# Optimization experiments

Measured on AMD Instinct MI355X. Metric: run time of the kernel, lower is better.

The kernel has to match this reference:

```python
import jax, jax.numpy as jnp
import numpy as np
import math

N = 50000
E = 800000
HID = 128
HEADS = 8
DK = HID // HEADS
EPS_LN = 1e-5


def setup_inputs() -> dict:
    key = jax.random.key(0)
    ks = jax.random.split(key, 20)
    s = 1.0 / math.sqrt(HID)
    inp = {
        'x': jax.random.normal(ks[0], (N, HID), jnp.float32),
        'Wq': jax.random.normal(ks[1], (HID, HID), jnp.float32) * s,
        'bq': jnp.zeros((HID,), jnp.float32),
        'Wk': jax.random.normal(ks[2], (HID, HID), jnp.float32) * s,
        'bk': jnp.zeros((HID,), jnp.float32),
        'Wv': jax.random.normal(ks[3], (HID, HID), jnp.float32) * s,
        'bv': jnp.zeros((HID,), jnp.float32),
        'Wo': jax.random.normal(ks[4], (HID, HID), jnp.float32) * s,
        'bo': jnp.zeros((HID,), jnp.float32),
        'ln1_g': jnp.ones((HID,), jnp.float32),
        'ln1_b': jnp.zeros((HID,), jnp.float32),
        'W1': jax.random.normal(ks[5], (HID, 4 * HID), jnp.float32) * s,
        'b1': jnp.zeros((4 * HID,), jnp.float32),
        'W2': jax.random.normal(ks[6], (4 * HID, HID), jnp.float32) * (0.5 * s),
        'b2': jnp.zeros((HID,), jnp.float32),
        'ln2_g': jnp.ones((HID,), jnp.float32),
        'ln2_b': jnp.zeros((HID,), jnp.float32),
        'edge_index': jax.random.randint(ks[7], (2, E), 0, N, jnp.int64 if jax.config.jax_enable_x64 else jnp.int32),
    }
    return inp


def _layer_norm(x, g, b):
    mu = jnp.mean(x, axis=-1, keepdims=True)
    var = jnp.mean(jnp.square(x - mu), axis=-1, keepdims=True)
    return (x - mu) * jax.lax.rsqrt(var + EPS_LN) * g + b


def reference(x, Wq, bq, Wk, bk, Wv, bv, Wo, bo, ln1_g, ln1_b, W1, b1, W2, b2, ln2_g, ln2_b, edge_index):
    n = x.shape[0]
    src, tgt = edge_index[0], edge_index[1]
    Q = (x @ Wq + bq).reshape(n, HEADS, DK)
    K = (x @ Wk + bk).reshape(n, HEADS, DK)
    V = (x @ Wv + bv).reshape(n, HEADS, DK)
    # per-edge scores: (E, H)
    scores = jnp.sum(Q[tgt] * K[src], axis=-1) / math.sqrt(DK)
    # segment softmax over incoming edges of each target node
    smax = jax.ops.segment_max(scores, tgt, num_segments=n)  # (N, H), -inf for empty
    sexp = jnp.exp(scores - smax[tgt])
    ssum = jax.ops.segment_sum(sexp, tgt, num_segments=n)
    alpha = sexp / (ssum[tgt] + 1e-16)  # (E, H)
    # weighted V aggregation
    messages = alpha[:, :, None] * V[src]  # (E, H, DK)
    agg = jax.ops.segment_sum(messages, tgt, num_segments=n).reshape(n, HID)
    out = agg @ Wo + bo
    h = _layer_norm(x + out, ln1_g, ln1_b)
    ff = jax.nn.relu(h @ W1 + b1) @ W2 + b2
    return _layer_norm(h + ff, ln2_g, ln2_b)
```

## Files before the change

### kernel.cpp

```cpp
#include <hip/hip_runtime.h>
#include <math.h>

typedef __attribute__((ext_vector_type(8))) short bf16x8;
typedef __attribute__((ext_vector_type(4))) float f32x4;

__device__ __forceinline__ unsigned short f2b(float f) {
    unsigned int u = __float_as_uint(f);
    unsigned int r = (u + 0x7fffu + ((u >> 16) & 1u)) >> 16;
    return (unsigned short)r;
}
__device__ __forceinline__ float blo(unsigned int w) { return __uint_as_float(w << 16); }
__device__ __forceinline__ float bhi(unsigned int w) { return __uint_as_float(w & 0xffff0000u); }
__device__ __forceinline__ float b2f(unsigned short u) { return __uint_as_float((unsigned int)u << 16); }

__device__ __forceinline__ void gload_lds16(const void* g, void* lds) {
    __builtin_amdgcn_global_load_lds(
        (const __attribute__((address_space(1))) unsigned int*)g,
        (__attribute__((address_space(3))) unsigned int*)lds, 16, 0, 0);
}

template<int K, int EPI>
__global__ __launch_bounds__(256)
void mfma_gemm(const unsigned short* __restrict__ A,
               const unsigned short* __restrict__ BT,
               const float* __restrict__ bias,
               const void* __restrict__ res,
               const float* __restrict__ lng,
               const float* __restrict__ lnb,
               void* __restrict__ outv, int M, int NC)
{
    __shared__ unsigned short As[128 * 64];
    __shared__ unsigned short Bs[128 * 64];
    const int tid  = threadIdx.x;
    const int lane = tid & 63;
    const int wid  = tid >> 6;
    const int wr = wid >> 1, wc = wid & 1;
    const int rowBase = blockIdx.x * 128;
    const int colBase = blockIdx.y * 128;

    f32x4 acc[4][4];
#pragma unroll
    for (int i = 0; i < 4; ++i)
#pragma unroll
        for (int j = 0; j < 4; ++j) acc[i][j] = (f32x4)0.f;

    int srow[4], skoff[4];
#pragma unroll
    for (int t = 0; t < 4; ++t) {
        int c = tid + t * 256;
        int r = c >> 3, cc = c & 7;
        srow[t]  = r;
        skoff[t] = ((cc ^ (r & 7)) << 3);
    }

    const int rl = lane & 15;
    const int kh = lane >> 4;

    for (int k0 = 0; k0 < K; k0 += 64) {
#pragma unroll
        for (int t = 0; t < 4; ++t) {
            int c = tid + t * 256;
            gload_lds16(A + (size_t)(rowBase + srow[t]) * K + k0 + skoff[t], &As[c * 8]);
            gload_lds16(BT + (size_t)(colBase + srow[t]) * K + k0 + skoff[t], &Bs[c * 8]);
        }
        __syncthreads();

        bf16x8 a[4][2], b[4][2];
#pragma unroll
        for (int mi = 0; mi < 4; ++mi)
#pragma unroll
            for (int kt = 0; kt < 2; ++kt) {
                a[mi][kt] = *(const bf16x8*)&As[(((wr * 64 + mi * 16 + rl) * 64) + kt * 32 + kh * 8) ^ ((rl & 7) << 3)];
                b[mi][kt] = *(const bf16x8*)&Bs[(((wc * 64 + mi * 16 + rl) * 64) + kt * 32 + kh * 8) ^ ((rl & 7) << 3)];
            }
#pragma unroll
        for (int kt = 0; kt < 2; ++kt)
#pragma unroll
            for (int mi = 0; mi < 4; ++mi)
#pragma unroll
                for (int ni = 0; ni < 4; ++ni)
                    acc[mi][ni] = __builtin_amdgcn_mfma_f32_16x16x32_bf16(a[mi][kt], b[ni][kt], acc[mi][ni], 0, 0, 0);
        __syncthreads();
    }

    if (EPI == 3 || EPI == 4) {
        float* ls = (float*)As;
        float bb[4], gg[4], be[4];
#pragma unroll
        for (int ni = 0; ni < 4; ++ni) {
            int col = wc * 64 + ni * 16 + rl;
            bb[ni] = bias[col];
            gg[ni] = lng[col];
            be[ni] = lnb[col];
        }
#pragma unroll
        for (int mi = 0; mi < 4; ++mi) {
#pragma unroll
            for (int r = 0; r < 4; ++r) {
                int lrow = wr * 64 + mi * 16 + kh * 4 + r;
                int row  = rowBase + lrow;
                float s = 0.f, ss = 0.f;
#pragma unroll
                for (int ni = 0; ni < 4; ++ni) {
                    int col = wc * 64 + ni * 16 + rl;
                    float rr = 0.f;
                    if (row < M) {
                        if (EPI == 3) rr = ((const float*)res)[(size_t)row * 128 + col];
                        else          rr = b2f(((const unsigned short*)res)[(size_t)row * 128 + col]);
                    }
                    float v = acc[mi][ni][r] + bb[ni] + rr;
                    acc[mi][ni][r] = v;
                    s += v; ss += v * v;
                }
#pragma unroll
                for (int off = 1; off < 16; off <<= 1) {
                    s  += __shfl_xor(s,  off, 64);
                    ss += __shfl_xor(ss, off, 64);
                }
                if (rl == 0) {
                    ls[lrow * 2 + wc]       = s;
                    ls[256 + lrow * 2 + wc] = ss;
                }
            }
        }
        __syncthreads();
#pragma unroll
        for (int mi = 0; mi < 4; ++mi) {
#pragma unroll
            for (int r = 0; r < 4; ++r) {
                int lrow = wr * 64 + mi * 16 + kh * 4 + r;
                int row  = rowBase + lrow;
                float s  = ls[lrow * 2] + ls[lrow * 2 + 1];
                float ss = ls[256 + lrow * 2] + ls[256 + lrow * 2 + 1];
                float mean = s * (1.f / 128.f);
                float var  = ss * (1.f / 128.f) - mean * mean;
                float rstd = rsqrtf(var + 1e-5f);
#pragma unroll
                for (int ni = 0; ni < 4; ++ni) {
                    int col = wc * 64 + ni * 16 + rl;
                    float o = (acc[mi][ni][r] - mean) * rstd * gg[ni] + be[ni];
                    if (EPI == 3) {
                        ((unsigned short*)outv)[(size_t)row * 128 + col] = (row < M) ? f2b(o) : (unsigned short)0;
                    } else {
                        if (row < M) ((float*)outv)[(size_t)row * 128 + col] = o;
                    }
                }
            }
        }
    } else {
#pragma unroll
        for (int ni = 0; ni < 4; ++ni) {
            const int col = colBase + wc * 64 + ni * 16 + rl;
            const float bv = bias[col];
#pragma unroll
            for (int mi = 0; mi < 4; ++mi) {
                const int rowb = rowBase + wr * 64 + mi * 16 + kh * 4;
#pragma unroll
                for (int r = 0; r < 4; ++r) {
                    float v = acc[mi][ni][r] + bv;
                    if (EPI == 1) v = fmaxf(v, 0.f);
                    ((unsigned short*)outv)[(size_t)(rowb + r) * NC + col] = f2b(v);
                }
            }
        }
    }
}

__global__ void cast_all(const float* __restrict__ x, unsigned short* __restrict__ xb,
                         int n, int npad, int xblocks,
                         const float* __restrict__ Wq, const float* __restrict__ Wk,
                         const float* __restrict__ Wv, const float* __restrict__ Wo,
                         const float* __restrict__ W1, const float* __restrict__ W2,
                         const float* __restrict__ bq, const float* __restrict__ bk,
                         const float* __restrict__ bv,
                         unsigned short* __restrict__ WcatT, unsigned short* __restrict__ WoT,
                         unsigned short* __restrict__ W1T, unsigned short* __restrict__ W2T,
                         float* __restrict__ bqkv, int* __restrict__ bcnt)
{
    if (blockIdx.x < (unsigned)xblocks) {
        size_t i = ((size_t)blockIdx.x * 256 + threadIdx.x) * 4;
        if (i >= (size_t)npad * 128) return;
        float4 v = make_float4(0.f, 0.f, 0.f, 0.f);
        if (i < (size_t)n * 128) v = *(const float4*)(x + i);
        ushort4 o;
        o.x = f2b(v.x); o.y = f2b(v.y); o.z = f2b(v.z); o.w = f2b(v.w);
        *(ushort4*)(xb + i) = o;
        return;
    }
    int i = (blockIdx.x - xblocks) * 256 + threadIdx.x;
    if (i < 49152) {
        int j = i >> 7, k = i & 127;
        const float* W = (j < 128) ? Wq : ((j < 256) ? Wk : Wv);
        WcatT[i] = f2b(W[k * 128 + (j & 127)]);
    } else if (i < 65536) {
        int t = i - 49152; int j = t >> 7, k = t & 127;
        WoT[t] = f2b(Wo[k * 128 + j]);
    } else if (i < 131072) {
        int t = i - 65536; int j = t >> 7, k = t & 127;
        W1T[t] = f2b(W1[k * 512 + j]);
    } else if (i < 196608) {
        int t = i - 131072; int j = t >> 9, k = t & 511;
        W2T[t] = f2b(W2[k * 128 + j]);
    }
    if (i < 384) bqkv[i] = (i < 128) ? bq[i] : ((i < 256) ? bk[i - 128] : bv[i - 256]);
    if (i < 1024) bcnt[i] = 0;
}

#define EPB 8192

__global__ __launch_bounds__(512)
void bucket_count(const int* __restrict__ tgt, int* __restrict__ bcnt, int E, int nb)
{
    __shared__ int hist[1024];
    int base = blockIdx.x * EPB;
    for (int i = threadIdx.x; i < nb; i += 512) hist[i] = 0;
    __syncthreads();
    int end = min(base + EPB, E);
    for (int e = base + threadIdx.x; e < end; e += 512)
        atomicAdd(&hist[tgt[e] >> 6], 1);
    __syncthreads();
    for (int i = threadIdx.x; i < nb; i += 512)
        if (hist[i] > 0) atomicAdd(&bcnt[i], hist[i]);
}

__global__ __launch_bounds__(64)
void bucket_scan(const int* __restrict__ bcnt, int* __restrict__ bstart,
                 int* __restrict__ bcur, int nb, int E)
{
    int lane = threadIdx.x;
    int carry = 0;
    for (int c = 0; c < nb; c += 64) {
        int idx = c + lane;
        int v = (idx < nb) ? bcnt[idx] : 0;
        int orig = v;
#pragma unroll
        for (int off = 1; off < 64; off <<= 1) {
            int y = __shfl_up(v, off, 64);
            if (lane >= off) v += y;
        }
        if (idx < nb) { int ex = carry + v - orig; bstart[idx] = ex; bcur[idx] = ex; }
        carry += __shfl(v, 63, 64);
    }
    if (lane == 0) bstart[nb] = E;
}

__global__ __launch_bounds__(512)
void bucket_group(const int* __restrict__ src, const int* __restrict__ tgt,
                  int* __restrict__ bcur, int2* __restrict__ stage, int E, int nb)
{
    __shared__ int2 eb[EPB];
    __shared__ int hist[1024], lofs[1024], lcur[1024], gbase[1024];
    int base = blockIdx.x * EPB;
    int tid = threadIdx.x;
    for (int i = tid; i < nb; i += 512) { hist[i] = 0; lcur[i] = 0; }
    __syncthreads();
    int end = min(base + EPB, E);
    for (int e = base + tid; e < end; e += 512)
        atomicAdd(&hist[tgt[e] >> 6], 1);
    __syncthreads();
    if (tid < 64) {
        int carry = 0;
        for (int c = 0; c < nb; c += 64) {
            int idx = c + tid;
            int v = (idx < nb) ? hist[idx] : 0;
            int orig = v;
#pragma unroll
            for (int off = 1; off < 64; off <<= 1) {
                int y = __shfl_up(v, off, 64);
                if (tid >= off) v += y;
            }
            if (idx < nb) lofs[idx] = carry + v - orig;
            carry += __shfl(v, 63, 64);
        }
    }
    __syncthreads();
    for (int e = base + tid; e < end; e += 512) {
        int t = tgt[e], b = t >> 6;
        int r = atomicAdd(&lcur[b], 1);
        eb[lofs[b] + r] = make_int2(src[e], t);
    }
    __syncthreads();
    for (int i = tid; i < nb; i += 512)
        if (hist[i] > 0) gbase[i] = atomicAdd(&bcur[i], hist[i]);
    __syncthreads();
    int cnt = end - base;
    for (int i = tid; i < cnt; i += 512) {
        int2 v = eb[i];
        int b = v.y >> 6;
        stage[gbase[b] + (i - lofs[b])] = v;
    }
}

__global__ __launch_bounds__(256)
void bucket_sort(const int2* __restrict__ stage, const int* __restrict__ bstart,
                 int* __restrict__ rowp, int2* __restrict__ epos, int n, int nb)
{
    __shared__ int2 eb[3072], eb2[3072];
    __shared__ int tcnt[64], tofs[64], tcur[64];
    int b = blockIdx.x;
    int t0 = b << 6;
    if (t0 >= n) return;
    int t1 = min(t0 + 64, n);
    int s0 = bstart[b], s1 = bstart[b + 1];
    int cnt = s1 - s0;
    int tid = threadIdx.x;
    if (tid < 64) { tcnt[tid] = 0; tcur[tid] = 0; }
    __syncthreads();
    bool fits = (cnt <= 3072);
    if (fits) {
        for (int i = tid; i < cnt; i += 256) {
            int2 v = stage[s0 + i];
            eb[i] = v;
            atomicAdd(&tcnt[v.y - t0], 1);
        }
    } else {
        for (int i = tid; i < cnt; i += 256)
            atomicAdd(&tcnt[stage[s0 + i].y - t0], 1);
    }
    __syncthreads();
    if (tid < 64) {
        int v = tcnt[tid], orig = v;
#pragma unroll
        for (int off = 1; off < 64; off <<= 1) {
            int y = __shfl_up(v, off, 64);
            if (tid >= off) v += y;
        }
        tofs[tid] = v - orig;
        int t = t0 + tid;
        if (t < t1) rowp[t] = s0 + v - orig;
        if (t == n - 1) rowp[n] = s1;
    }
    __syncthreads();
    if (fits) {
        for (int i = tid; i < cnt; i += 256) {
            int2 v = eb[i];
            int lt = v.y - t0;
            int r = atomicAdd(&tcur[lt], 1);
            eb2[tofs[lt] + r] = v;
        }
        __syncthreads();
        for (int i = tid; i < cnt; i += 256) epos[s0 + i] = eb2[i];
    } else {
        for (int i = tid; i < cnt; i += 256) {
            int2 v = stage[s0 + i];
            int lt = v.y - t0;
            int r = atomicAdd(&tcur[lt], 1);
            epos[s0 + tofs[lt] + r] = v;
        }
    }
}

#define SCORE_SCALE 0.360673760222241f

__global__ __launch_bounds__(256)
void score_kernel(const unsigned short* __restrict__ qkv, const int2* __restrict__ epos,
                  float* __restrict__ scores, int E)
{
    int gw = (blockIdx.x * 256 + threadIdx.x) >> 4;
    int el = threadIdx.x & 15;
    if (gw >= E) return;
    int2 st = epos[gw];
    uint4 qv = *(const uint4*)(qkv + (size_t)st.y * 384 + el * 8);
    uint4 kv = *(const uint4*)(qkv + (size_t)st.x * 384 + 128 + el * 8);
    float d;
    d  = blo(qv.x) * blo(kv.x) + bhi(qv.x) * bhi(kv.x);
    d += blo(qv.y) * blo(kv.y) + bhi(qv.y) * bhi(kv.y);
    d += blo(qv.z) * blo(kv.z) + bhi(qv.z) * bhi(kv.z);
    d += blo(qv.w) * blo(kv.w) + bhi(qv.w) * bhi(kv.w);
    d += __shfl_xor(d, 1, 64);
    if ((el & 1) == 0)
        scores[(size_t)gw * 8 + (el >> 1)] = d * SCORE_SCALE;
}

__global__ __launch_bounds__(256)
void softmax_kernel(const int* __restrict__ rowp, const float* __restrict__ sc,
                    unsigned short* __restrict__ wbf, int n)
{
    int b = blockIdx.x;
#pragma unroll
    for (int pp = 0; pp < 2; ++pp) {
        int p = threadIdx.x + pp * 256;
        int lt = p >> 3, h = p & 7;
        int t = (b << 6) + lt;
        if (t >= n) continue;
        int e0 = rowp[t], e1 = rowp[t + 1];
        if (e0 >= e1) continue;
        float m = -INFINITY;
        for (int e = e0; e < e1; ++e) m = fmaxf(m, sc[(size_t)e * 8 + h]);
        float s = 0.f;
        for (int e = e0; e < e1; ++e) s += exp2f(sc[(size_t)e * 8 + h] - m);
        float inv = 1.f / (s + 1e-16f);
        for (int e = e0; e < e1; ++e)
            wbf[(size_t)e * 8 + h] = f2b(exp2f(sc[(size_t)e * 8 + h] - m) * inv);
    }
}

__global__ __launch_bounds__(256)
void attn_agg(const unsigned short* __restrict__ qkv, const int* __restrict__ rowp,
              const int2* __restrict__ epos, const unsigned short* __restrict__ wbf,
              unsigned short* __restrict__ agg, int n, int npad)
{
    int wid  = (blockIdx.x * blockDim.x + threadIdx.x) >> 6;
    int lane = threadIdx.x & 63;
    if (wid >= npad) return;
    if (wid >= n) { *(unsigned int*)(agg + (size_t)wid * 128 + lane * 2) = 0u; return; }

    const int head = lane >> 3;
    int e = rowp[wid];
    const int e1 = rowp[wid + 1];

    float a0 = 0.f, a1 = 0.f;

    for (; e + 4 <= e1; e += 4) {
        int s0 = epos[e].x, s1 = epos[e + 1].x, s2 = epos[e + 2].x, s3 = epos[e + 3].x;
        float w0 = b2f(wbf[(size_t)e * 8 + head]);
        float w1 = b2f(wbf[(size_t)(e + 1) * 8 + head]);
        float w2 = b2f(wbf[(size_t)(e + 2) * 8 + head]);
        float w3 = b2f(wbf[(size_t)(e + 3) * 8 + head]);
        unsigned int v0 = *(const unsigned int*)(qkv + (size_t)s0 * 384 + 256 + lane * 2);
        unsigned int v1 = *(const unsigned int*)(qkv + (size_t)s1 * 384 + 256 + lane * 2);
        unsigned int v2 = *(const unsigned int*)(qkv + (size_t)s2 * 384 + 256 + lane * 2);
        unsigned int v3 = *(const unsigned int*)(qkv + (size_t)s3 * 384 + 256 + lane * 2);
        a0 += (w0 * blo(v0) + w1 * blo(v1)) + (w2 * blo(v2) + w3 * blo(v3));
        a1 += (w0 * bhi(v0) + w1 * bhi(v1)) + (w2 * bhi(v2) + w3 * bhi(v3));
    }
    for (; e < e1; ++e) {
        int s = epos[e].x;
        float w = b2f(wbf[(size_t)e * 8 + head]);
        unsigned int vw = *(const unsigned int*)(qkv + (size_t)s * 384 + 256 + lane * 2);
        a0 += w * blo(vw);
        a1 += w * bhi(vw);
    }
    unsigned int o = (unsigned int)f2b(a0) | ((unsigned int)f2b(a1) << 16);
    *(unsigned int*)(agg + (size_t)wid * 128 + lane * 2) = o;
}

extern "C" void kernel_launch(void* const* d_in, const int* in_sizes, int n_in,
                              void* d_out, int out_size, void* d_ws, size_t ws_size,
                              hipStream_t stream)
{
    const float* x    = (const float*)d_in[0];
    const float* Wq   = (const float*)d_in[1];
    const float* bq   = (const float*)d_in[2];
    const float* Wk   = (const float*)d_in[3];
    const float* bk   = (const float*)d_in[4];
    const float* Wv   = (const float*)d_in[5];
    const float* bv   = (const float*)d_in[6];
    const float* Wo   = (const float*)d_in[7];
    const float* bo   = (const float*)d_in[8];
    const float* ln1g = (const float*)d_in[9];
    const float* ln1b = (const float*)d_in[10];
    const float* W1   = (const float*)d_in[11];
    const float* b1   = (const float*)d_in[12];
    const float* W2   = (const float*)d_in[13];
    const float* b2   = (const float*)d_in[14];
    const float* ln2g = (const float*)d_in[15];
    const float* ln2b = (const float*)d_in[16];
    const int*   eidx = (const int*)d_in[17];

    const int N_ = in_sizes[0] / 128;
    const int E_ = in_sizes[17] / 2;
    const int Mpad = ((N_ + 127) / 128) * 128;
    const int nb = (N_ + 63) >> 6;
    const int* srcE = eidx;
    const int* tgtE = eidx + E_;
    float* out = (float*)d_out;

    unsigned short* xb   = (unsigned short*)d_ws;
    unsigned short* qkvb = xb + (size_t)Mpad * 128;
    unsigned short* tb   = xb;
    unsigned short* wbf  = xb;
    unsigned short* aggb = qkvb + (size_t)Mpad * 384;
    unsigned short* hb   = aggb + (size_t)Mpad * 128;
    float* scores        = (float*)(hb + (size_t)Mpad * 128);
    unsigned short* WcatT = (unsigned short*)(scores + (size_t)E_ * 8);
    unsigned short* WoT  = WcatT + 384 * 128;
    unsigned short* W1T  = WoT + 128 * 128;
    unsigned short* W2T  = W1T + 512 * 128;
    float* bqkv          = (float*)(W2T + 128 * 512);
    int2* stage          = (int2*)(bqkv + 384);
    int2* epos           = stage + E_;
    int* bcnt   = (int*)(epos + E_);
    int* bstart = bcnt + 1024;
    int* bcur   = bstart + 1025;
    int* rowp   = bcur + 1024;

    const int xblocks = (int)(((size_t)Mpad * 128 / 4 + 255) / 256);
    const int gblocks = (E_ + EPB - 1) / EPB;

    cast_all<<<xblocks + 768, 256, 0, stream>>>(x, xb, N_, Mpad, xblocks,
                                                Wq, Wk, Wv, Wo, W1, W2, bq, bk, bv,
                                                WcatT, WoT, W1T, W2T, bqkv, bcnt);

    mfma_gemm<128, 2><<<dim3(Mpad / 128, 3), 256, 0, stream>>>(
        xb, WcatT, bqkv, nullptr, nullptr, nullptr, qkvb, N_, 384);

    bucket_count<<<gblocks, 512, 0, stream>>>(tgtE, bcnt, E_, nb);
    bucket_scan<<<1, 64, 0, stream>>>(bcnt, bstart, bcur, nb, E_);
    bucket_group<<<gblocks, 512, 0, stream>>>(srcE, tgtE, bcur, stage, E_, nb);
    bucket_sort<<<nb, 256, 0, stream>>>(stage, bstart, rowp, epos, N_, nb);

    score_kernel<<<((size_t)E_ * 16 + 255) / 256, 256, 0, stream>>>(qkvb, epos, scores, E_);
    softmax_kernel<<<nb, 256, 0, stream>>>(rowp, scores, wbf, N_);
    attn_agg<<<(Mpad + 3) / 4, 256, 0, stream>>>(qkvb, rowp, epos, wbf, aggb, N_, Mpad);

    mfma_gemm<128, 3><<<dim3(Mpad / 128, 1), 256, 0, stream>>>(
        aggb, WoT, bo, x, ln1g, ln1b, hb, N_, 128);

    mfma_gemm<128, 1><<<dim3(Mpad / 128, 4), 256, 0, stream>>>(
        hb, W1T, b1, nullptr, nullptr, nullptr, tb, N_, 512);

    mfma_gemm<512, 4><<<dim3(Mpad / 128, 1), 256, 0, stream>>>(
        tb, W2T, b2, hb, ln2g, ln2b, out, N_, 128);
}
```

Measured before the change: 242.6 us.

## Fuse segment softmax into attention aggregation with online max/sum

Removes the separate softmax kernel. Each wavefront in attn_agg now computes the per-head running max and sum over its target's incoming edges using an online softmax with shuffle reductions. It then recomputes the exp weights on the fly from the fp32 scores and normalises the accumulated result once at the end. This avoids a kernel launch, the three-pass scan over scores and the bf16 weight write and re-read, at the cost of extra exp work and a second read of scores inside the aggregation kernel.

```diff
diff --git a/kernel.cpp b/kernel.cpp
--- a/kernel.cpp
+++ b/kernel.cpp
@@ -373,31 +373,8 @@
 }
 
 __global__ __launch_bounds__(256)
-void softmax_kernel(const int* __restrict__ rowp, const float* __restrict__ sc,
-                    unsigned short* __restrict__ wbf, int n)
-{
-    int b = blockIdx.x;
-#pragma unroll
-    for (int pp = 0; pp < 2; ++pp) {
-        int p = threadIdx.x + pp * 256;
-        int lt = p >> 3, h = p & 7;
-        int t = (b << 6) + lt;
-        if (t >= n) continue;
-        int e0 = rowp[t], e1 = rowp[t + 1];
-        if (e0 >= e1) continue;
-        float m = -INFINITY;
-        for (int e = e0; e < e1; ++e) m = fmaxf(m, sc[(size_t)e * 8 + h]);
-        float s = 0.f;
-        for (int e = e0; e < e1; ++e) s += exp2f(sc[(size_t)e * 8 + h] - m);
-        float inv = 1.f / (s + 1e-16f);
-        for (int e = e0; e < e1; ++e)
-            wbf[(size_t)e * 8 + h] = f2b(exp2f(sc[(size_t)e * 8 + h] - m) * inv);
-    }
-}
-
-__global__ __launch_bounds__(256)
 void attn_agg(const unsigned short* __restrict__ qkv, const int* __restrict__ rowp,
-              const int2* __restrict__ epos, const unsigned short* __restrict__ wbf,
+              const int2* __restrict__ epos, const float* __restrict__ sc,
               unsigned short* __restrict__ agg, int n, int npad)
 {
     int wid  = (blockIdx.x * blockDim.x + threadIdx.x) >> 6;
@@ -405,18 +382,37 @@
     if (wid >= npad) return;
     if (wid >= n) { *(unsigned int*)(agg + (size_t)wid * 128 + lane * 2) = 0u; return; }
 
+    const int e0 = rowp[wid];
+    const int e1 = rowp[wid + 1];
+
+    const int h1 = lane & 7;
+    float m = -1e30f, s = 0.f;
+    for (int e = e0 + (lane >> 3); e < e1; e += 8) {
+        float v = sc[(size_t)e * 8 + h1];
+        float mn = fmaxf(m, v);
+        s = s * exp2f(m - mn) + exp2f(v - mn);
+        m = mn;
+    }
+#pragma unroll
+    for (int off = 8; off < 64; off <<= 1) {
+        float mo = __shfl_xor(m, off, 64);
+        float so = __shfl_xor(s, off, 64);
+        float mn = fmaxf(m, mo);
+        s = s * exp2f(m - mn) + so * exp2f(mo - mn);
+        m = mn;
+    }
     const int head = lane >> 3;
-    int e = rowp[wid];
-    const int e1 = rowp[wid + 1];
+    const float M   = __shfl(m, head, 64);
+    const float inv = 1.f / (__shfl(s, head, 64) + 1e-16f);
 
     float a0 = 0.f, a1 = 0.f;
-
+    int e = e0;
     for (; e + 4 <= e1; e += 4) {
         int s0 = epos[e].x, s1 = epos[e + 1].x, s2 = epos[e + 2].x, s3 = epos[e + 3].x;
-        float w0 = b2f(wbf[(size_t)e * 8 + head]);
-        float w1 = b2f(wbf[(size_t)(e + 1) * 8 + head]);
-        float w2 = b2f(wbf[(size_t)(e + 2) * 8 + head]);
-        float w3 = b2f(wbf[(size_t)(e + 3) * 8 + head]);
+        float w0 = exp2f(sc[(size_t)e * 8 + head] - M);
+        float w1 = exp2f(sc[(size_t)(e + 1) * 8 + head] - M);
+        float w2 = exp2f(sc[(size_t)(e + 2) * 8 + head] - M);
+        float w3 = exp2f(sc[(size_t)(e + 3) * 8 + head] - M);
         unsigned int v0 = *(const unsigned int*)(qkv + (size_t)s0 * 384 + 256 + lane * 2);
         unsigned int v1 = *(const unsigned int*)(qkv + (size_t)s1 * 384 + 256 + lane * 2);
         unsigned int v2 = *(const unsigned int*)(qkv + (size_t)s2 * 384 + 256 + lane * 2);
@@ -425,12 +421,13 @@
         a1 += (w0 * bhi(v0) + w1 * bhi(v1)) + (w2 * bhi(v2) + w3 * bhi(v3));
     }
     for (; e < e1; ++e) {
-        int s = epos[e].x;
-        float w = b2f(wbf[(size_t)e * 8 + head]);
-        unsigned int vw = *(const unsigned int*)(qkv + (size_t)s * 384 + 256 + lane * 2);
+        int sx = epos[e].x;
+        float w = exp2f(sc[(size_t)e * 8 + head] - M);
+        unsigned int vw = *(const unsigned int*)(qkv + (size_t)sx * 384 + 256 + lane * 2);
         a0 += w * blo(vw);
         a1 += w * bhi(vw);
     }
+    a0 *= inv; a1 *= inv;
     unsigned int o = (unsigned int)f2b(a0) | ((unsigned int)f2b(a1) << 16);
     *(unsigned int*)(agg + (size_t)wid * 128 + lane * 2) = o;
 }
@@ -469,7 +466,6 @@
     unsigned short* xb   = (unsigned short*)d_ws;
     unsigned short* qkvb = xb + (size_t)Mpad * 128;
     unsigned short* tb   = xb;
-    unsigned short* wbf  = xb;
     unsigned short* aggb = qkvb + (size_t)Mpad * 384;
     unsigned short* hb   = aggb + (size_t)Mpad * 128;
     float* scores        = (float*)(hb + (size_t)Mpad * 128);
@@ -501,8 +497,7 @@
     bucket_sort<<<nb, 256, 0, stream>>>(stage, bstart, rowp, epos, N_, nb);
 
     score_kernel<<<((size_t)E_ * 16 + 255) / 256, 256, 0, stream>>>(qkvb, epos, scores, E_);
-    softmax_kernel<<<nb, 256, 0, stream>>>(rowp, scores, wbf, N_);
-    attn_agg<<<(Mpad + 3) / 4, 256, 0, stream>>>(qkvb, rowp, epos, wbf, aggb, N_, Mpad);
+    attn_agg<<<(Mpad + 3) / 4, 256, 0, stream>>>(qkvb, rowp, epos, scores, aggb, N_, Mpad);
 
     mfma_gemm<128, 3><<<dim3(Mpad / 128, 1), 256, 0, stream>>>(
         aggb, WoT, bo, x, ln1g, ln1b, hb, N_, 128);
```

Measured after the change: 222.9 us. -8.1%, faster.
